# Kernel tuning notes

Measured on AMD Instinct MI355X. Metric: run time of the kernel, lower is better.

## Reference

```python
import jax, jax.numpy as jnp
import numpy as np

N, E, G = 200000, 1200000, 2048
NODE_DIM, H = 5, 64
NEG_SLOPE = 0.2


def setup_inputs() -> dict:
    key = jax.random.key(0)
    ks = jax.random.split(key, 20)
    def glorot(k, shape):
        fan = sum(shape) if len(shape) > 1 else shape[0] + 1
        return jax.random.normal(k, shape, jnp.float32) * jnp.sqrt(2.0 / fan)
    inp = {
        'x': jax.random.normal(ks[0], (N, NODE_DIM), jnp.float32),
        'edge_index': jax.random.randint(ks[1], (2, E), 0, N, jnp.int64),
        'batch': jnp.sort(jax.random.randint(ks[2], (N,), 0, G, jnp.int64)),
        'embed_W': glorot(ks[3], (NODE_DIM, H)), 'embed_b': jnp.zeros((H,), jnp.float32),
        'g1_W': glorot(ks[4], (H, H)), 'g1_asrc': glorot(ks[5], (H,)), 'g1_adst': glorot(ks[6], (H,)), 'g1_b': jnp.zeros((H,), jnp.float32),
        'g2_W': glorot(ks[7], (H, H)), 'g2_asrc': glorot(ks[8], (H,)), 'g2_adst': glorot(ks[9], (H,)), 'g2_b': jnp.zeros((H,), jnp.float32),
        'fc1_W': glorot(ks[10], (2 * H, 64)), 'fc1_b': jnp.zeros((64,), jnp.float32),
        'fc2_W': glorot(ks[11], (64, 32)), 'fc2_b': jnp.zeros((32,), jnp.float32),
        'fc3_W': glorot(ks[12], (32, 1)), 'fc3_b': jnp.zeros((1,), jnp.float32),
    }
    return inp


def gat_conv(x, src, dst, W, a_src, a_dst, b):
    # x: [N, H] -> h: [N, H]; edges (with self-loops) src->dst
    h = x @ W
    alpha_s = h @ a_src  # [N]
    alpha_d = h @ a_dst  # [N]
    e = jax.nn.leaky_relu(alpha_s[src] + alpha_d[dst], NEG_SLOPE)  # [E']
    m = jax.ops.segment_max(e, dst, num_segments=N)
    w = jnp.exp(e - m[dst])
    denom = jax.ops.segment_sum(w, dst, num_segments=N)
    alpha = w / (denom[dst] + 1e-16)
    out = jax.ops.segment_sum(h[src] * alpha[:, None], dst, num_segments=N)
    return out + b


def reference(x, edge_index, batch, embed_W, embed_b,
              g1_W, g1_asrc, g1_adst, g1_b,
              g2_W, g2_asrc, g2_adst, g2_b,
              fc1_W, fc1_b, fc2_W, fc2_b, fc3_W, fc3_b):
    # add self loops once (PyG GATConv default add_self_loops=True)
    loops = jnp.arange(N, dtype=edge_index.dtype)
    src = jnp.concatenate([edge_index[0], loops])
    dst = jnp.concatenate([edge_index[1], loops])

    h = x @ embed_W + embed_b
    h = gat_conv(h, src, dst, g1_W, g1_asrc, g1_adst, g1_b)
    h = jax.nn.relu(h)
    h = gat_conv(h, src, dst, g2_W, g2_asrc, g2_adst, g2_b)

    # global mean / max pooling per graph
    cnt = jax.ops.segment_sum(jnp.ones((N,), h.dtype), batch, num_segments=G)
    mean = jax.ops.segment_sum(h, batch, num_segments=G) / jnp.maximum(cnt, 1.0)[:, None]
    mx = jax.ops.segment_max(h, batch, num_segments=G)
    mx = jnp.where(cnt[:, None] > 0, mx, 0.0)
    g = jnp.concatenate([mean, mx], axis=1)  # [G, 2H]

    g = jax.nn.relu(g @ fc1_W + fc1_b)
    g = jax.nn.relu(g @ fc2_W + fc2_b)
    return g @ fc3_W + fc3_b  # [G, 1]
```

## Files before the change

### kernel.cpp

```cpp
#include <hip/hip_runtime.h>
#include <hip/hip_bf16.h>
#include <hip/hip_fp16.h>

#define HD 64
#define NODE_DIM 5
#define NEG_SLOPE 0.2f
#define GT 64
#define BSH 9
#define BNODES 512
#define NBMAX 512
#define BCAP 4096
#define EPB 8

template <bool EMBED>
__global__ __launch_bounds__(256) void gemm_alpha_k(
    const void* __restrict__ hin, const float* __restrict__ embW,
    const float* __restrict__ embB, const float* __restrict__ W,
    const float* __restrict__ asrc, const float* __restrict__ adst,
    __half* __restrict__ hout, float* __restrict__ alpha_s,
    float* __restrict__ alpha_d, int N) {
    __shared__ float hs[GT][HD + 1];
    __shared__ float Ws[HD * HD];
    __shared__ float xe[GT * NODE_DIM];
    __shared__ float we[NODE_DIM * HD + HD];
    const int t = threadIdx.x;
    const int n0 = blockIdx.x * GT;
    if (n0 >= N) return;
    const int rem = N - n0;

    {
        const float4* w4 = (const float4*)W;
        float4* s4 = (float4*)Ws;
#pragma unroll
        for (int j = 0; j < 4; j++) s4[t + 256 * j] = w4[t + 256 * j];
    }
    if (EMBED) {
        const float* xin = (const float*)hin;
        for (int j = t; j < GT * NODE_DIM; j += 256)
            xe[j] = (j < rem * NODE_DIM) ? xin[(size_t)n0 * NODE_DIM + j] : 0.0f;
        for (int j = t; j < NODE_DIM * HD + HD; j += 256)
            we[j] = (j < NODE_DIM * HD) ? embW[j] : embB[j - NODE_DIM * HD];
        __syncthreads();
        int r = t >> 2, d0 = (t & 3) * 16;
#pragma unroll
        for (int jj = 0; jj < 16; jj++) {
            int d = d0 + jj;
            float acc = we[NODE_DIM * HD + d];
#pragma unroll
            for (int k = 0; k < NODE_DIM; k++)
                acc = fmaf(xe[r * NODE_DIM + k], we[k * HD + d], acc);
            hs[r][d] = (r < rem) ? acc : 0.0f;
        }
    } else {
        const short4* g4 = (const short4*)((const __half*)hin + (size_t)n0 * HD);
#pragma unroll
        for (int j = 0; j < 4; j++) {
            int idx = t + 256 * j;
            int row = idx >> 4, c4 = idx & 15;
            short4 v = {0, 0, 0, 0};
            if (row < rem) v = g4[idx];
            hs[row][c4 * 4 + 0] = __half2float(__short_as_half(v.x));
            hs[row][c4 * 4 + 1] = __half2float(__short_as_half(v.y));
            hs[row][c4 * 4 + 2] = __half2float(__short_as_half(v.z));
            hs[row][c4 * 4 + 3] = __half2float(__short_as_half(v.w));
        }
    }
    __syncthreads();

    const int dq = t & 15;
    const int grp = t >> 4;
    float4 acc[4];
#pragma unroll
    for (int i = 0; i < 4; i++) acc[i] = {0, 0, 0, 0};

#pragma unroll 8
    for (int k = 0; k < 64; k++) {
        float4 w4 = *(const float4*)(Ws + k * HD + dq * 4);
#pragma unroll
        for (int i = 0; i < 4; i++) {
            float hv = hs[grp * 4 + i][k];
            acc[i].x = fmaf(hv, w4.x, acc[i].x);
            acc[i].y = fmaf(hv, w4.y, acc[i].y);
            acc[i].z = fmaf(hv, w4.z, acc[i].z);
            acc[i].w = fmaf(hv, w4.w, acc[i].w);
        }
    }

    float4 a4 = ((const float4*)asrc)[dq];
    float4 b4 = ((const float4*)adst)[dq];
#pragma unroll
    for (int i = 0; i < 4; i++) {
        int n = n0 + grp * 4 + i;
        if (n >= N) break;
        short4 s;
        s.x = __half_as_short(__float2half_rn(acc[i].x));
        s.y = __half_as_short(__float2half_rn(acc[i].y));
        s.z = __half_as_short(__float2half_rn(acc[i].z));
        s.w = __half_as_short(__float2half_rn(acc[i].w));
        ((short4*)hout)[(size_t)n * 16 + dq] = s;
        float ps = acc[i].x * a4.x + acc[i].y * a4.y + acc[i].z * a4.z + acc[i].w * a4.w;
        float pd = acc[i].x * b4.x + acc[i].y * b4.y + acc[i].z * b4.z + acc[i].w * b4.w;
#pragma unroll
        for (int off = 8; off; off >>= 1) {
            ps += __shfl_xor(ps, off);
            pd += __shfl_xor(pd, off);
        }
        if (dq == 0) {
            alpha_s[n] = ps;
            alpha_d[n] = pd;
        }
    }
}


__global__ void zero_k(int* __restrict__ p, int total) {
    int i = blockIdx.x * blockDim.x + threadIdx.x;
    if (i < total) p[i] = 0;
}

__global__ __launch_bounds__(256) void partition_k(
    const int* __restrict__ ei, int* __restrict__ bcnt,
    int* __restrict__ bpack, int E) {
    __shared__ int lcnt[NBMAX], lbase[NBMAX];
    int dst[EPB], src[EPB];
    int jb = blockIdx.x * (256 * EPB) + threadIdx.x;
#pragma unroll
    for (int u = 0; u < EPB; u++) {
        int j = jb + u * 256;
        if (j < E) {
            dst[u] = __builtin_nontemporal_load(&ei[E + j]);
            src[u] = __builtin_nontemporal_load(&ei[j]);
        } else dst[u] = -1;
    }
    for (int b = threadIdx.x; b < NBMAX; b += 256) lcnt[b] = 0;
    __syncthreads();
#pragma unroll
    for (int u = 0; u < EPB; u++)
        if (dst[u] >= 0) atomicAdd(&lcnt[dst[u] >> BSH], 1);
    __syncthreads();
    for (int b = threadIdx.x; b < NBMAX; b += 256) {
        int c = lcnt[b];
        lbase[b] = c ? (b * BCAP + atomicAdd(&bcnt[b], c)) : 0;
        lcnt[b] = 0;
    }
    __syncthreads();
#pragma unroll
    for (int u = 0; u < EPB; u++) {
        if (dst[u] >= 0) {
            int b = dst[u] >> BSH;
            int o = atomicAdd(&lcnt[b], 1);
            bpack[lbase[b] + o] = (src[u] << BSH) | (dst[u] & (BNODES - 1));
        }
    }
}

__global__ void bucket_scan_k(const int* __restrict__ bcnt,
                              int* __restrict__ bbase, int NB) {
    __shared__ int s[NBMAX];
    int t = threadIdx.x;
    int v = (t < NB) ? bcnt[t] : 0;
    s[t] = v;
    __syncthreads();
#pragma unroll
    for (int o = 1; o < NBMAX; o <<= 1) {
        int tv = (t >= o) ? s[t - o] : 0;
        __syncthreads();
        s[t] += tv;
        __syncthreads();
    }
    if (t < NB) {
        bbase[t] = s[t] - v;
        if (t == NB - 1) bbase[NB] = s[t];
    }
}

__global__ __launch_bounds__(256) void bucket_csr_k(
    const int* __restrict__ bpack, const int* __restrict__ bcnt,
    const int* __restrict__ bbase,
    int* __restrict__ off, int* __restrict__ csr_src, int N) {
    __shared__ int s[BNODES];
    __shared__ int lcur[BNODES];
    const int t = threadIdx.x;
    const int b = blockIdx.x;
    const int nbase = b << BSH;
    const int cnt = bcnt[b];
    const int w0 = b * BCAP;
    const int e0 = bbase[b];

    s[t] = 0; s[t + 256] = 0;
    __syncthreads();
    for (int j = t; j < cnt; j += 256)
        atomicAdd(&s[bpack[w0 + j] & (BNODES - 1)], 1);
    __syncthreads();
    int d0 = s[t], d1 = s[t + 256];
#pragma unroll
    for (int o = 1; o < BNODES; o <<= 1) {
        int a0 = (t >= o) ? s[t - o] : 0;
        int a1 = (t + 256 >= o) ? s[t + 256 - o] : 0;
        __syncthreads();
        s[t] += a0;
        s[t + 256] += a1;
        __syncthreads();
    }
    int ex0 = s[t] - d0, ex1 = s[t + 256] - d1;
    lcur[t] = ex0; lcur[t + 256] = ex1;
    int n0 = nbase + t, n1 = nbase + t + 256;
    if (n0 < N) off[n0] = e0 + ex0;
    if (n1 < N) off[n1] = e0 + ex1;
    if (t == 255 && b == gridDim.x - 1) off[N] = e0 + cnt;
    __syncthreads();
    for (int j = t; j < cnt; j += 256) {
        int v = bpack[w0 + j];
        int pos = atomicAdd(&lcur[v & (BNODES - 1)], 1);
        csr_src[e0 + pos] = v >> BSH;
    }
}

template <bool BR>
__global__ __launch_bounds__(256) void gather_k(
    const int* __restrict__ off, const int* __restrict__ csr_src,
    const float* __restrict__ as, const float* __restrict__ ad,
    const __half* __restrict__ h, const float* __restrict__ bias,
    __half* __restrict__ out, int N) {
    int tid = blockIdx.x * blockDim.x + threadIdx.x;
    int wv = tid >> 6;
    int lane = threadIdx.x & 63;
    int grp = lane >> 4;
    int l16 = lane & 15;
    int n = wv * 4 + grp;
    if (n >= N) return;
    int s0 = off[n], s1 = off[n + 1];
    float adv = ad[n];
    const short4* h4 = (const short4*)h;

    float e = as[n] + adv;
    e = (e >= 0.0f) ? e : NEG_SLOPE * e;
    float wsl = __expf(e);
    float l0 = wsl, l1 = 0.0f;
    short4 hvs = h4[(unsigned)(n * 16 + l16)];
    float4 acc0, acc1 = {0, 0, 0, 0};
    acc0.x = wsl * __half2float(__short_as_half(hvs.x));
    acc0.y = wsl * __half2float(__short_as_half(hvs.y));
    acc0.z = wsl * __half2float(__short_as_half(hvs.z));
    acc0.w = wsl * __half2float(__short_as_half(hvs.w));

    int i = s0;
    for (; i + 4 <= s1; i += 4) {
        int src0 = csr_src[i], src1 = csr_src[i + 1];
        int src2 = csr_src[i + 2], src3 = csr_src[i + 3];
        float e0 = as[src0] + adv, e1 = as[src1] + adv;
        float e2 = as[src2] + adv, e3 = as[src3] + adv;
        short4 hv0 = h4[(unsigned)(src0 * 16 + l16)];
        short4 hv1 = h4[(unsigned)(src1 * 16 + l16)];
        short4 hv2 = h4[(unsigned)(src2 * 16 + l16)];
        short4 hv3 = h4[(unsigned)(src3 * 16 + l16)];
        e0 = (e0 >= 0.0f) ? e0 : NEG_SLOPE * e0;
        e1 = (e1 >= 0.0f) ? e1 : NEG_SLOPE * e1;
        e2 = (e2 >= 0.0f) ? e2 : NEG_SLOPE * e2;
        e3 = (e3 >= 0.0f) ? e3 : NEG_SLOPE * e3;
        float w0 = __expf(e0), w1 = __expf(e1), w2 = __expf(e2), w3 = __expf(e3);
        l0 += w0 + w2; l1 += w1 + w3;
        acc0.x = fmaf(w0, __half2float(__short_as_half(hv0.x)), acc0.x);
        acc0.y = fmaf(w0, __half2float(__short_as_half(hv0.y)), acc0.y);
        acc0.z = fmaf(w0, __half2float(__short_as_half(hv0.z)), acc0.z);
        acc0.w = fmaf(w0, __half2float(__short_as_half(hv0.w)), acc0.w);
        acc1.x = fmaf(w1, __half2float(__short_as_half(hv1.x)), acc1.x);
        acc1.y = fmaf(w1, __half2float(__short_as_half(hv1.y)), acc1.y);
        acc1.z = fmaf(w1, __half2float(__short_as_half(hv1.z)), acc1.z);
        acc1.w = fmaf(w1, __half2float(__short_as_half(hv1.w)), acc1.w);
        acc0.x = fmaf(w2, __half2float(__short_as_half(hv2.x)), acc0.x);
        acc0.y = fmaf(w2, __half2float(__short_as_half(hv2.y)), acc0.y);
        acc0.z = fmaf(w2, __half2float(__short_as_half(hv2.z)), acc0.z);
        acc0.w = fmaf(w2, __half2float(__short_as_half(hv2.w)), acc0.w);
        acc1.x = fmaf(w3, __half2float(__short_as_half(hv3.x)), acc1.x);
        acc1.y = fmaf(w3, __half2float(__short_as_half(hv3.y)), acc1.y);
        acc1.z = fmaf(w3, __half2float(__short_as_half(hv3.z)), acc1.z);
        acc1.w = fmaf(w3, __half2float(__short_as_half(hv3.w)), acc1.w);
    }
    for (; i + 2 <= s1; i += 2) {
        int src0 = csr_src[i], src1 = csr_src[i + 1];
        float e0 = as[src0] + adv;
        float e1 = as[src1] + adv;
        short4 hv0 = h4[(unsigned)(src0 * 16 + l16)];
        short4 hv1 = h4[(unsigned)(src1 * 16 + l16)];
        e0 = (e0 >= 0.0f) ? e0 : NEG_SLOPE * e0;
        e1 = (e1 >= 0.0f) ? e1 : NEG_SLOPE * e1;
        float w0 = __expf(e0), w1 = __expf(e1);
        l0 += w0; l1 += w1;
        acc0.x = fmaf(w0, __half2float(__short_as_half(hv0.x)), acc0.x);
        acc0.y = fmaf(w0, __half2float(__short_as_half(hv0.y)), acc0.y);
        acc0.z = fmaf(w0, __half2float(__short_as_half(hv0.z)), acc0.z);
        acc0.w = fmaf(w0, __half2float(__short_as_half(hv0.w)), acc0.w);
        acc1.x = fmaf(w1, __half2float(__short_as_half(hv1.x)), acc1.x);
        acc1.y = fmaf(w1, __half2float(__short_as_half(hv1.y)), acc1.y);
        acc1.z = fmaf(w1, __half2float(__short_as_half(hv1.z)), acc1.z);
        acc1.w = fmaf(w1, __half2float(__short_as_half(hv1.w)), acc1.w);
    }
    if (i < s1) {
        int src0 = csr_src[i];
        float e0 = as[src0] + adv;
        short4 hv0 = h4[(unsigned)(src0 * 16 + l16)];
        e0 = (e0 >= 0.0f) ? e0 : NEG_SLOPE * e0;
        float w0 = __expf(e0);
        l0 += w0;
        acc0.x = fmaf(w0, __half2float(__short_as_half(hv0.x)), acc0.x);
        acc0.y = fmaf(w0, __half2float(__short_as_half(hv0.y)), acc0.y);
        acc0.z = fmaf(w0, __half2float(__short_as_half(hv0.z)), acc0.z);
        acc0.w = fmaf(w0, __half2float(__short_as_half(hv0.w)), acc0.w);
    }
    float inv = 1.0f / (l0 + l1 + 1e-16f);
    float4 r;
    r.x = (acc0.x + acc1.x) * inv;
    r.y = (acc0.y + acc1.y) * inv;
    r.z = (acc0.z + acc1.z) * inv;
    r.w = (acc0.w + acc1.w) * inv;
    if (BR) {
        float4 b = ((const float4*)bias)[l16];
        r.x = fmaxf(r.x + b.x, 0.0f);
        r.y = fmaxf(r.y + b.y, 0.0f);
        r.z = fmaxf(r.z + b.z, 0.0f);
        r.w = fmaxf(r.w + b.w, 0.0f);
    }
    short4 o;
    o.x = __half_as_short(__float2half_rn(r.x));
    o.y = __half_as_short(__float2half_rn(r.y));
    o.z = __half_as_short(__float2half_rn(r.z));
    o.w = __half_as_short(__float2half_rn(r.w));
    ((short4*)out)[(unsigned)(n * 16 + l16)] = o;
}

__global__ __launch_bounds__(256) void pool_mlp_k(
    const __half* __restrict__ hfin, const float* __restrict__ hb,
    const int* __restrict__ batch, int N,
    const float* __restrict__ fc1W, const float* __restrict__ fc1b,
    const float* __restrict__ fc2W, const float* __restrict__ fc2b,
    const float* __restrict__ fc3W, const float* __restrict__ fc3b,
    float* __restrict__ out) {
    __shared__ float psum[4][64];
    __shared__ float pmax[4][64];
    __shared__ float lds[192];
    int g = blockIdx.x;
    int lane = threadIdx.x & 63;
    int w = threadIdx.x >> 6;
    int lo = 0, hi = N;
    while (lo < hi) { int mid = (lo + hi) >> 1; if (batch[mid] < g) lo = mid + 1; else hi = mid; }
    int start = lo;
    lo = start; hi = N;
    while (lo < hi) { int mid = (lo + hi) >> 1; if (batch[mid] < g + 1) lo = mid + 1; else hi = mid; }
    int end = lo;
    float bias = hb[lane];
    float sum = 0.0f, mx = -INFINITY;
    for (int n = start + w; n < end; n += 4) {
        float v = __half2float(hfin[(size_t)n * HD + lane]) + bias;
        sum += v;
        mx = fmaxf(mx, v);
    }
    psum[w][lane] = sum;
    pmax[w][lane] = mx;
    __syncthreads();
    if (w == 0) {
        int cnt = end - start;
        float s = psum[0][lane] + psum[1][lane] + psum[2][lane] + psum[3][lane];
        float m = fmaxf(fmaxf(pmax[0][lane], pmax[1][lane]),
                        fmaxf(pmax[2][lane], pmax[3][lane]));
        lds[lane] = (cnt > 0) ? s / (float)cnt : 0.0f;
        lds[64 + lane] = (cnt > 0) ? m : 0.0f;
    }
    __syncthreads();
    if (w == 0) {
        float o1 = fc1b[lane];
        for (int k = 0; k < 128; k++) o1 += lds[k] * fc1W[k * 64 + lane];
        o1 = fmaxf(o1, 0.0f);
        __builtin_amdgcn_s_barrier();
        lds[128 + lane] = o1;
        float o2 = 0.0f;
        if (lane < 32) {
            o2 = fc2b[lane];
            for (int k = 0; k < 64; k++) o2 += lds[128 + k] * fc2W[k * 32 + lane];
            o2 = fmaxf(o2, 0.0f);
        }
        float part = (lane < 32) ? o2 * fc3W[lane] : 0.0f;
#pragma unroll
        for (int off = 32; off; off >>= 1) part += __shfl_xor(part, off);
        if (lane == 0) out[g] = part + fc3b[0];
    }
}

static inline size_t align256(size_t x) { return (x + 255) & ~(size_t)255; }

extern "C" void kernel_launch(void* const* d_in, const int* in_sizes, int n_in,
                              void* d_out, int out_size, void* d_ws, size_t ws_size,
                              hipStream_t stream) {
    const float* x      = (const float*)d_in[0];
    const int*   ei     = (const int*)d_in[1];
    const int*   batch  = (const int*)d_in[2];
    const float* embW   = (const float*)d_in[3];
    const float* embB   = (const float*)d_in[4];
    const float* g1W    = (const float*)d_in[5];
    const float* g1as   = (const float*)d_in[6];
    const float* g1ad   = (const float*)d_in[7];
    const float* g1b    = (const float*)d_in[8];
    const float* g2W    = (const float*)d_in[9];
    const float* g2as   = (const float*)d_in[10];
    const float* g2ad   = (const float*)d_in[11];
    const float* g2b    = (const float*)d_in[12];
    const float* fc1W   = (const float*)d_in[13];
    const float* fc1b   = (const float*)d_in[14];
    const float* fc2W   = (const float*)d_in[15];
    const float* fc2b   = (const float*)d_in[16];
    const float* fc3W   = (const float*)d_in[17];
    const float* fc3b   = (const float*)d_in[18];
    float* out = (float*)d_out;

    const int N  = in_sizes[0] / NODE_DIM;
    const int E  = in_sizes[1] / 2;
    const int G  = out_size;
    const int NH = N * HD;
    const int NB = (N + BNODES - 1) >> BSH;

    char* ws = (char*)d_ws;
    __half* bufA    = (__half*)ws; ws += align256((size_t)NH * 2);
    __half* bufB    = (__half*)ws; ws += align256((size_t)NH * 2);
    float*  as_buf  = (float*)ws;  ws += align256((size_t)N * 4);
    float*  ad_buf  = (float*)ws;  ws += align256((size_t)N * 4);
    int*    off     = (int*)ws;    ws += align256((size_t)(N + 1) * 4);
    int*    bcnt    = (int*)ws;    ws += align256((size_t)NBMAX * 4);
    int*    bbase   = (int*)ws;    ws += align256((size_t)(NBMAX + 1) * 4);
    int*    bpack   = (int*)ws;    ws += align256((size_t)NB * BCAP * 4);
    int*    csrsrc  = (int*)ws;    ws += align256((size_t)E * 4);

    const int B = 256;
    dim3 blk(B);
    dim3 gr_gemm((N + GT - 1) / GT);
    dim3 gr_gath(((N + 3) / 4 * 64 + B - 1) / B);
    dim3 gr_epb((E + B * EPB - 1) / (B * EPB));
    dim3 gr_n((N + B - 1) / B);

    zero_k<<<dim3(2), blk, 0, stream>>>(bcnt, NBMAX);
    partition_k<<<gr_epb, blk, 0, stream>>>(ei, bcnt, bpack, E);
    bucket_scan_k<<<dim3(1), dim3(NBMAX), 0, stream>>>(bcnt, bbase, NB);
    bucket_csr_k<<<dim3(NB), blk, 0, stream>>>(bpack, bcnt, bbase, off, csrsrc, N);

    gemm_alpha_k<true><<<gr_gemm, blk, 0, stream>>>(x, embW, embB, g1W, g1as, g1ad,
                                                    bufB, as_buf, ad_buf, N);
    gather_k<true><<<gr_gath, blk, 0, stream>>>(off, csrsrc, as_buf, ad_buf,
                                                bufB, g1b, bufA, N);

    gemm_alpha_k<false><<<gr_gemm, blk, 0, stream>>>(bufA, nullptr, nullptr, g2W,
                                                     g2as, g2ad, bufB, as_buf, ad_buf, N);
    gather_k<false><<<gr_gath, blk, 0, stream>>>(off, csrsrc, as_buf, ad_buf,
                                                 bufB, nullptr, bufA, N);

    pool_mlp_k<<<dim3(G), dim3(256), 0, stream>>>(bufA, g2b, batch, N,
                                                  fc1W, fc1b, fc2W, fc2b, fc3W, fc3b, out);
}
```

Before: 304.0 us.

## Use MFMA fp16 matrix instructions for node projection GEMM

Replaces the scalar FMA 64x64 node projection with MFMA 16x16x32 fp16 instructions. W is transposed into padded fp16 shared memory, and the input tile stays fp16 in shared memory. The alpha projections are reduced across lane groups. The aim is to cut VALU work and LDS traffic in the GEMM kernel, at the cost of rounding the embed output and W to fp16 before the multiply.

After: 277.7 us. 1.09x faster.

```diff
diff --git a/kernel.cpp b/kernel.cpp
--- a/kernel.cpp
+++ b/kernel.cpp
@@ -11,6 +11,10 @@
 #define NBMAX 512
 #define BCAP 4096
 #define EPB 8
+#define LDH 72
+
+typedef _Float16 f16x8 __attribute__((ext_vector_type(8)));
+typedef float f32x4 __attribute__((ext_vector_type(4)));
 
 template <bool EMBED>
 __global__ __launch_bounds__(256) void gemm_alpha_k(
@@ -19,8 +23,8 @@
     const float* __restrict__ asrc, const float* __restrict__ adst,
     __half* __restrict__ hout, float* __restrict__ alpha_s,
     float* __restrict__ alpha_d, int N) {
-    __shared__ float hs[GT][HD + 1];
-    __shared__ float Ws[HD * HD];
+    __shared__ _Float16 hs[GT * LDH];
+    __shared__ _Float16 Wt[HD * LDH];
     __shared__ float xe[GT * NODE_DIM];
     __shared__ float we[NODE_DIM * HD + HD];
     const int t = threadIdx.x;
@@ -28,12 +32,13 @@
     if (n0 >= N) return;
     const int rem = N - n0;
 
-    {
-        const float4* w4 = (const float4*)W;
-        float4* s4 = (float4*)Ws;
-#pragma unroll
-        for (int j = 0; j < 4; j++) s4[t + 256 * j] = w4[t + 256 * j];
-    }
+#pragma unroll
+    for (int j = 0; j < 16; j++) {
+        int idx = t + 256 * j;
+        int k = idx >> 6, n = idx & 63;
+        Wt[n * LDH + k] = (_Float16)W[idx];
+    }
+
     if (EMBED) {
         const float* xin = (const float*)hin;
         for (int j = t; j < GT * NODE_DIM; j += 256)
@@ -49,7 +54,7 @@
 #pragma unroll
             for (int k = 0; k < NODE_DIM; k++)
                 acc = fmaf(xe[r * NODE_DIM + k], we[k * HD + d], acc);
-            hs[r][d] = (r < rem) ? acc : 0.0f;
+            hs[r * LDH + d] = (r < rem) ? (_Float16)acc : (_Float16)0.0f;
         }
     } else {
         const short4* g4 = (const short4*)((const __half*)hin + (size_t)n0 * HD);
@@ -59,56 +64,59 @@
             int row = idx >> 4, c4 = idx & 15;
             short4 v = {0, 0, 0, 0};
             if (row < rem) v = g4[idx];
-            hs[row][c4 * 4 + 0] = __half2float(__short_as_half(v.x));
-            hs[row][c4 * 4 + 1] = __half2float(__short_as_half(v.y));
-            hs[row][c4 * 4 + 2] = __half2float(__short_as_half(v.z));
-            hs[row][c4 * 4 + 3] = __half2float(__short_as_half(v.w));
+            *(short4*)(hs + row * LDH + c4 * 4) = v;
         }
     }
     __syncthreads();
 
-    const int dq = t & 15;
-    const int grp = t >> 4;
-    float4 acc[4];
-#pragma unroll
-    for (int i = 0; i < 4; i++) acc[i] = {0, 0, 0, 0};
-
-#pragma unroll 8
-    for (int k = 0; k < 64; k++) {
-        float4 w4 = *(const float4*)(Ws + k * HD + dq * 4);
-#pragma unroll
-        for (int i = 0; i < 4; i++) {
-            float hv = hs[grp * 4 + i][k];
-            acc[i].x = fmaf(hv, w4.x, acc[i].x);
-            acc[i].y = fmaf(hv, w4.y, acc[i].y);
-            acc[i].z = fmaf(hv, w4.z, acc[i].z);
-            acc[i].w = fmaf(hv, w4.w, acc[i].w);
+    const int lane = t & 63;
+    const int w = t >> 6;
+    const int r16 = lane & 15;
+    const int g = lane >> 4;
+
+    const _Float16* hrow = hs + (w * 16 + r16) * LDH + g * 8;
+    f16x8 b0 = *(const f16x8*)(hrow);
+    f16x8 b1 = *(const f16x8*)(hrow + 32);
+
+    f32x4 acc[4];
+#pragma unroll
+    for (int mt = 0; mt < 4; mt++) acc[mt] = (f32x4){0.f, 0.f, 0.f, 0.f};
+
+#pragma unroll
+    for (int mt = 0; mt < 4; mt++) {
+        const _Float16* arow = Wt + (mt * 16 + r16) * LDH + g * 8;
+        f16x8 a0 = *(const f16x8*)(arow);
+        f16x8 a1 = *(const f16x8*)(arow + 32);
+        acc[mt] = __builtin_amdgcn_mfma_f32_16x16x32_f16(a0, b0, acc[mt], 0, 0, 0);
+        acc[mt] = __builtin_amdgcn_mfma_f32_16x16x32_f16(a1, b1, acc[mt], 0, 0, 0);
+    }
+
+    const int node = n0 + w * 16 + r16;
+    float ps = 0.0f, pd = 0.0f;
+    if (node < N) {
+#pragma unroll
+        for (int mt = 0; mt < 4; mt++) {
+            float4 av = ((const float4*)asrc)[mt * 4 + g];
+            float4 bv = ((const float4*)adst)[mt * 4 + g];
+            ps += acc[mt][0] * av.x + acc[mt][1] * av.y +
+                  acc[mt][2] * av.z + acc[mt][3] * av.w;
+            pd += acc[mt][0] * bv.x + acc[mt][1] * bv.y +
+                  acc[mt][2] * bv.z + acc[mt][3] * bv.w;
+            short4 s;
+            s.x = __half_as_short(__float2half_rn(acc[mt][0]));
+            s.y = __half_as_short(__float2half_rn(acc[mt][1]));
+            s.z = __half_as_short(__float2half_rn(acc[mt][2]));
+            s.w = __half_as_short(__float2half_rn(acc[mt][3]));
+            ((short4*)hout)[(size_t)node * 16 + mt * 4 + g] = s;
         }
     }
-
-    float4 a4 = ((const float4*)asrc)[dq];
-    float4 b4 = ((const float4*)adst)[dq];
-#pragma unroll
-    for (int i = 0; i < 4; i++) {
-        int n = n0 + grp * 4 + i;
-        if (n >= N) break;
-        short4 s;
-        s.x = __half_as_short(__float2half_rn(acc[i].x));
-        s.y = __half_as_short(__float2half_rn(acc[i].y));
-        s.z = __half_as_short(__float2half_rn(acc[i].z));
-        s.w = __half_as_short(__float2half_rn(acc[i].w));
-        ((short4*)hout)[(size_t)n * 16 + dq] = s;
-        float ps = acc[i].x * a4.x + acc[i].y * a4.y + acc[i].z * a4.z + acc[i].w * a4.w;
-        float pd = acc[i].x * b4.x + acc[i].y * b4.y + acc[i].z * b4.z + acc[i].w * b4.w;
-#pragma unroll
-        for (int off = 8; off; off >>= 1) {
-            ps += __shfl_xor(ps, off);
-            pd += __shfl_xor(pd, off);
-        }
-        if (dq == 0) {
-            alpha_s[n] = ps;
-            alpha_d[n] = pd;
-        }
+    ps += __shfl_xor(ps, 16);
+    ps += __shfl_xor(ps, 32);
+    pd += __shfl_xor(pd, 16);
+    pd += __shfl_xor(pd, 32);
+    if (g == 0 && node < N) {
+        alpha_s[node] = ps;
+        alpha_d[node] = pd;
     }
 }
 
```
